# Optimization experiments

Hardware: AMD Instinct MI355X
Metric: run time of the kernel (lower is better)

The kernel has to match this reference:

```python
import jax, jax.numpy as jnp
import numpy as np

EMB = 4096   # emb_size for c2=256 (per TransformerEncoderBlock mapping)
HEADS = 16
HDIM = EMB // HEADS  # 256
N = 25               # (h // (h//5))**2 patches
PATCH = 4            # h//5 with h=20
C = 256
HW = 20
LN_EPS = 1e-5


def _layernorm(x, g, b):
    m = jnp.mean(x, axis=-1, keepdims=True)
    v = jnp.var(x, axis=-1, keepdims=True)
    return (x - m) * jax.lax.rsqrt(v + LN_EPS) * g + b


def setup_inputs() -> dict:
    key = jax.random.key(0)
    ks = jax.random.split(key, 14)
    s = 0.02
    rn = lambda k, shape, sc=s: jax.random.normal(k, shape, jnp.float32) * sc
    return {
        "x": jax.random.normal(ks[0], (1, C, HW, HW), jnp.float32),
        # PatchEmbedding: Conv2d(C, EMB, k=4, s=4) + positions
        "pe_w": rn(ks[1], (EMB, C, PATCH, PATCH)),
        "pe_b": jnp.zeros((EMB,), jnp.float32),
        "pos": rn(ks[2], (N, EMB), 1.0),  # nn.Parameter(torch.randn(...))
        # shared LayerNorm (same module used twice per block)
        "ln_g": jnp.ones((EMB,), jnp.float32),
        "ln_b": jnp.zeros((EMB,), jnp.float32),
        # attention
        "qkv_w": rn(ks[3], (EMB, 3 * EMB)),
        "qkv_b": jnp.zeros((3 * EMB,), jnp.float32),
        "proj_w": rn(ks[4], (EMB, EMB)),
        "proj_b": jnp.zeros((EMB,), jnp.float32),
        # FFN (expansion 4)
        "ff1_w": rn(ks[5], (EMB, 4 * EMB)),
        "ff1_b": jnp.zeros((4 * EMB,), jnp.float32),
        "ff2_w": rn(ks[6], (4 * EMB, EMB)),
        "ff2_b": jnp.zeros((EMB,), jnp.float32),
    }


def _forward(x, pe_w, pe_b, pos, ln_g, ln_b, qkv_w, qkv_b, proj_w, proj_b,
             ff1_w, ff1_b, ff2_w, ff2_b):
    b = x.shape[0]
    # Patch embedding: Conv2d(k=4, s=4) -> [b, EMB, 5, 5] -> [b, 25, EMB]
    t = jax.lax.conv_general_dilated(
        x, pe_w, window_strides=(PATCH, PATCH), padding="VALID",
        dimension_numbers=("NCHW", "OIHW", "NCHW"))
    t = t + pe_b[None, :, None, None]
    t = t.reshape(b, EMB, N).transpose(0, 2, 1) + pos  # [b, N, EMB]

    # --- TransformerEncoderBlock (dropout inactive / eval mode) ---
    # attention branch
    h = _layernorm(t, ln_g, ln_b)
    qkv = (h @ qkv_w + qkv_b).reshape(b, N, HEADS, HDIM, 3)  # (h d qkv) split
    q = qkv[..., 0].transpose(0, 2, 1, 3)  # [b, H, N, D]
    k = qkv[..., 1].transpose(0, 2, 1, 3)
    v = qkv[..., 2].transpose(0, 2, 1, 3)
    energy = jnp.einsum("bhqd,bhkd->bhqk", q, k)
    # NOTE: original scales AFTER softmax by sqrt(emb_size) -- faithful copy
    att = jax.nn.softmax(energy, axis=-1) / (EMB ** 0.5)
    o = jnp.einsum("bhqk,bhkd->bhqd", att, v)
    o = o.transpose(0, 2, 1, 3).reshape(b, N, EMB)
    t = t + (o @ proj_w + proj_b)

    # FFN branch (same shared layernorm params)
    h = _layernorm(t, ln_g, ln_b)
    h = jax.nn.gelu(h @ ff1_w + ff1_b, approximate=False)  # torch nn.GELU exact
    t = t + (h @ ff2_w + ff2_b)

    # final reshape(1, c2, w, h)
    return t.reshape(1, C, HW, HW)


def reference(x, pe_w, pe_b, pos, ln_g, ln_b, qkv_w, qkv_b, proj_w, proj_b,
              ff1_w, ff1_b, ff2_w, ff2_b):
    return _forward(x, pe_w, pe_b, pos, ln_g, ln_b, qkv_w, qkv_b, proj_w,
                    proj_b, ff1_w, ff1_b, ff2_w, ff2_b)
```

## Files before the change

### kernel.cpp

```cpp
#include <hip/hip_runtime.h>
#include <math.h>

#define TOK 25

typedef __attribute__((ext_vector_type(8))) short short8_t;
typedef __attribute__((ext_vector_type(4))) float f32x4_t;
typedef __attribute__((ext_vector_type(8))) float floatx8;
typedef __attribute__((ext_vector_type(4))) float floatx4;
typedef __attribute__((ext_vector_type(8))) __bf16 bf16x8_t;
typedef __attribute__((ext_vector_type(4))) __bf16 bf16x4_t;

__device__ __forceinline__ short8_t cvt8(floatx8 f) {
  return __builtin_bit_cast(short8_t, __builtin_convertvector(f, bf16x8_t));
}
__device__ __forceinline__ uint2 cvt4pack(float4 v) {
  floatx4 f = {v.x, v.y, v.z, v.w};
  return __builtin_bit_cast(uint2, __builtin_convertvector(f, bf16x4_t));
}
__device__ __forceinline__ uint2 pack4(f32x4_t v) {
  floatx4 f = {v[0], v[1], v[2], v[3]};
  return __builtin_bit_cast(uint2, __builtin_convertvector(f, bf16x4_t));
}
__device__ __forceinline__ unsigned short bf1(float f) {
  return __builtin_bit_cast(unsigned short, (__bf16)f);
}


template <int KC, int WT, int G, int D>
__global__ __launch_bounds__(256) void k_mfma(
    const unsigned short* __restrict__ A, const float* __restrict__ W,
    uint2* __restrict__ part, int K, int N) {
  constexpr int LDA = KC + 8;
  constexpr int NS = KC / 32;
  __shared__ __align__(16) unsigned short As[TOK * LDA];
  const int tid = threadIdx.x;
  const int lane = tid & 63;
  const int lm = lane & 15;
  const int lg = lane >> 4;
  const int wv = tid >> 6;
  const int s = blockIdx.y;
  const int k0 = s * KC;
  const int c0 = blockIdx.x * (64 * G) + wv * (16 * G);
  for (int i = tid; i < TOK * (KC / 8); i += 256) {
    int r = i / (KC / 8);
    int o = i - r * (KC / 8);
    uint4 v = *reinterpret_cast<const uint4*>(A + (long)r * K + k0 + o * 8);
    *reinterpret_cast<uint4*>(&As[r * LDA + o * 8]) = v;
  }
  __syncthreads();
  const int r1 = 16 + lm;
  const int r1c = (r1 < TOK) ? r1 : 0;
  f32x4_t acc[G][2];
#pragma unroll
  for (int g = 0; g < G; ++g) {
    acc[g][0] = (f32x4_t){0.f, 0.f, 0.f, 0.f};
    acc[g][1] = (f32x4_t){0.f, 0.f, 0.f, 0.f};
  }
  auto loadW = [&](int ks, floatx8(&dst)[G]) {
    const int kb = k0 + ks + lg * 8;
    if (WT == 0) {
      const float* bp = W + (long)kb * N + c0 + lm;
#pragma unroll
      for (int j = 0; j < 8; ++j) {
        const float* bj = bp + (long)j * N;
#pragma unroll
        for (int g = 0; g < G; ++g) dst[g][j] = bj[g * 16];
      }
    } else {
#pragma unroll
      for (int g = 0; g < G; ++g) {
        const float* bp = W + (long)(c0 + g * 16 + lm) * K + kb;
        float4 b0 = *reinterpret_cast<const float4*>(bp);
        float4 b1 = *reinterpret_cast<const float4*>(bp + 4);
        dst[g] = (floatx8){b0.x, b0.y, b0.z, b0.w, b1.x, b1.y, b1.z, b1.w};
      }
    }
  };
  floatx8 wb[D + 1][G];
  loadW(0, wb[0]);
  if (D >= 2 && NS > 1) loadW(32, wb[1 % (D + 1)]);
#pragma unroll
  for (int st = 0; st < NS; ++st) {
    if (st + D < NS) loadW((st + D) * 32, wb[(st + D) % (D + 1)]);
    short8_t av0 =
        *reinterpret_cast<const short8_t*>(&As[lm * LDA + st * 32 + lg * 8]);
    short8_t av1 =
        *reinterpret_cast<const short8_t*>(&As[r1c * LDA + st * 32 + lg * 8]);
#pragma unroll
    for (int g = 0; g < G; ++g) {
      short8_t bv = cvt8(wb[st % (D + 1)][g]);
      acc[g][0] = __builtin_amdgcn_mfma_f32_16x16x32_bf16(av0, bv, acc[g][0], 0, 0, 0);
      acc[g][1] = __builtin_amdgcn_mfma_f32_16x16x32_bf16(av1, bv, acc[g][1], 0, 0, 0);
    }
  }
  const long sbase = (long)s * N * 8;
#pragma unroll
  for (int g = 0; g < G; ++g) {
    long t = ((long)(c0 >> 4) + g) * 128;
    part[sbase + t + lane] = pack4(acc[g][0]);
    part[sbase + t + 64 + lane] = pack4(acc[g][1]);
  }
}

template <int KC, int G, int D>
__global__ __launch_bounds__(256) void k_mfma_pe(
    const float* __restrict__ x, const float* __restrict__ W,
    uint2* __restrict__ part, int K, int N) {
  constexpr int LDA = KC + 8;
  constexpr int NS = KC / 32;
  __shared__ __align__(16) unsigned short As[TOK * LDA];
  const int tid = threadIdx.x;
  const int lane = tid & 63;
  const int lm = lane & 15;
  const int lg = lane >> 4;
  const int wv = tid >> 6;
  const int s = blockIdx.y;
  const int k0 = s * KC;
  const int c0 = blockIdx.x * (64 * G) + wv * (16 * G);
  for (int i = tid; i < TOK * (KC / 8); i += 256) {
    int r = i / (KC / 8);
    int o = i - r * (KC / 8);
    int kb = k0 + o * 8;
    int c = kb >> 4;
    int kh0 = (kb >> 2) & 3;
    int py = r / 5, px = r - py * 5;
    const float* xp = x + c * 400 + (py * 4 + kh0) * 20 + px * 4;
    float4 lo = *reinterpret_cast<const float4*>(xp);
    float4 hi = *reinterpret_cast<const float4*>(xp + 20);
    floatx8 f = {lo.x, lo.y, lo.z, lo.w, hi.x, hi.y, hi.z, hi.w};
    *reinterpret_cast<short8_t*>(&As[r * LDA + o * 8]) = cvt8(f);
  }
  __syncthreads();
  const int r1 = 16 + lm;
  const int r1c = (r1 < TOK) ? r1 : 0;
  f32x4_t acc[G][2];
#pragma unroll
  for (int g = 0; g < G; ++g) {
    acc[g][0] = (f32x4_t){0.f, 0.f, 0.f, 0.f};
    acc[g][1] = (f32x4_t){0.f, 0.f, 0.f, 0.f};
  }
  auto loadW = [&](int ks, floatx8(&dst)[G]) {
    const int kb = k0 + ks + lg * 8;
#pragma unroll
    for (int g = 0; g < G; ++g) {
      const float* bp = W + (long)(c0 + g * 16 + lm) * K + kb;
      float4 b0 = *reinterpret_cast<const float4*>(bp);
      float4 b1 = *reinterpret_cast<const float4*>(bp + 4);
      dst[g] = (floatx8){b0.x, b0.y, b0.z, b0.w, b1.x, b1.y, b1.z, b1.w};
    }
  };
  floatx8 wb[D + 1][G];
  loadW(0, wb[0]);
  if (D >= 2 && NS > 1) loadW(32, wb[1 % (D + 1)]);
#pragma unroll
  for (int st = 0; st < NS; ++st) {
    if (st + D < NS) loadW((st + D) * 32, wb[(st + D) % (D + 1)]);
    short8_t av0 =
        *reinterpret_cast<const short8_t*>(&As[lm * LDA + st * 32 + lg * 8]);
    short8_t av1 =
        *reinterpret_cast<const short8_t*>(&As[r1c * LDA + st * 32 + lg * 8]);
#pragma unroll
    for (int g = 0; g < G; ++g) {
      short8_t bv = cvt8(wb[st % (D + 1)][g]);
      acc[g][0] = __builtin_amdgcn_mfma_f32_16x16x32_bf16(av0, bv, acc[g][0], 0, 0, 0);
      acc[g][1] = __builtin_amdgcn_mfma_f32_16x16x32_bf16(av1, bv, acc[g][1], 0, 0, 0);
    }
  }
  const long sbase = (long)s * N * 8;
#pragma unroll
  for (int g = 0; g < G; ++g) {
    long t = ((long)(c0 >> 4) + g) * 128;
    part[sbase + t + lane] = pack4(acc[g][0]);
    part[sbase + t + 64 + lane] = pack4(acc[g][1]);
  }
}

template <int S, int GELU, int RES, int OBF>
__global__ __launch_bounds__(128) void k_reduce(const uint2* __restrict__ part,
                                                const float* __restrict__ bias,
                                                const float* __restrict__ res,
                                                void* __restrict__ outv,
                                                int Nout) {
  const long gidx = (long)blockIdx.x * 128 + threadIdx.x;
  const int lane = (int)(gidx & 63);
  const int half = (int)((gidx >> 6) & 1);
  const long ct = gidx >> 7;
  const int lm = lane & 15, lg = lane >> 4;
  const int col = (int)(ct * 16 + lm);
  const long stride = (long)Nout * 8;
  const uint2* pp = part + gidx;
  float a[4] = {0.f, 0.f, 0.f, 0.f};
#pragma unroll 16
  for (int s = 0; s < S; ++s) {
    uint2 u = pp[(long)s * stride];
    a[0] += __builtin_bit_cast(float, (u.x & 0xffffu) << 16);
    a[1] += __builtin_bit_cast(float, u.x & 0xffff0000u);
    a[2] += __builtin_bit_cast(float, (u.y & 0xffffu) << 16);
    a[3] += __builtin_bit_cast(float, u.y & 0xffff0000u);
  }
  const float bb = bias[col];
#pragma unroll
  for (int r = 0; r < 4; ++r) {
    a[r] += bb;
    if (GELU) a[r] = 0.5f * a[r] * (1.f + erff(a[r] * 0.70710678118654752f));
  }
  const int row0 = half * 16 + lg * 4;
#pragma unroll
  for (int r = 0; r < 4; ++r) {
    int row = row0 + r;
    if (row < TOK) {
      float v = a[r];
      if (RES) v += res[(long)row * Nout + col];
      if (OBF) {
        ((unsigned short*)outv)[(long)row * Nout + col] = bf1(v);
      } else {
        ((float*)outv)[(long)row * Nout + col] = v;
      }
    }
  }
}

__global__ __launch_bounds__(256) void k_ln(const float* __restrict__ t,
                                            const float* __restrict__ g,
                                            const float* __restrict__ b,
                                            unsigned short* __restrict__ h) {
  const int n = blockIdx.x;
  const float4* row = reinterpret_cast<const float4*>(t + n * 4096);
  float s = 0.f, s2 = 0.f;
  float4 vbuf[4];
#pragma unroll
  for (int it = 0; it < 4; ++it) {
    float4 v = row[threadIdx.x + it * 256];
    vbuf[it] = v;
    s += v.x + v.y + v.z + v.w;
    s2 += v.x * v.x + v.y * v.y + v.z * v.z + v.w * v.w;
  }
#pragma unroll
  for (int off = 32; off >= 1; off >>= 1) {
    s += __shfl_down(s, off);
    s2 += __shfl_down(s2, off);
  }
  __shared__ float red[8];
  if ((threadIdx.x & 63) == 0) {
    red[threadIdx.x >> 6] = s;
    red[4 + (threadIdx.x >> 6)] = s2;
  }
  __syncthreads();
  float st = red[0] + red[1] + red[2] + red[3];
  float s2t = red[4] + red[5] + red[6] + red[7];
  float mean = st * (1.f / 4096.f);
  float var = s2t * (1.f / 4096.f) - mean * mean;
  float rstd = rsqrtf(var + 1e-5f);
  const float4* g4 = reinterpret_cast<const float4*>(g);
  const float4* b4 = reinterpret_cast<const float4*>(b);
  uint2* h2 = reinterpret_cast<uint2*>(h) + (long)n * 1024;
#pragma unroll
  for (int it = 0; it < 4; ++it) {
    int i = threadIdx.x + it * 256;
    float4 v = vbuf[it];
    float4 gg = g4[i];
    float4 bb = b4[i];
    float4 o;
    o.x = (v.x - mean) * rstd * gg.x + bb.x;
    o.y = (v.y - mean) * rstd * gg.y + bb.y;
    o.z = (v.z - mean) * rstd * gg.z + bb.z;
    o.w = (v.w - mean) * rstd * gg.w + bb.w;
    h2[i] = cvt4pack(o);
  }
}

__global__ __launch_bounds__(256) void k_attn(const float* __restrict__ qkv,
                                              unsigned short* __restrict__ o) {
  const int head = blockIdx.x;
  __shared__ float q[TOK][260];
  __shared__ float kk[TOK][260];
  __shared__ float att[TOK][TOK];
  const int d = threadIdx.x;
#pragma unroll
  for (int n = 0; n < TOK; ++n) {
    const long base = (long)n * 12288 + (head * 256 + d) * 3;
    q[n][d] = qkv[base];
    kk[n][d] = qkv[base + 1];
  }
  __syncthreads();
  for (int p = threadIdx.x; p < TOK * TOK; p += 256) {
    int i = p / TOK, j = p - i * TOK;
    float acc = 0.f;
#pragma unroll
    for (int c = 0; c < 256; c += 4) {
      float4 a = *reinterpret_cast<const float4*>(&q[i][c]);
      float4 bb = *reinterpret_cast<const float4*>(&kk[j][c]);
      acc = fmaf(a.x, bb.x, acc);
      acc = fmaf(a.y, bb.y, acc);
      acc = fmaf(a.z, bb.z, acc);
      acc = fmaf(a.w, bb.w, acc);
    }
    att[i][j] = acc;
  }
  __syncthreads();
  if (threadIdx.x < TOK) {
    const int i = threadIdx.x;
    float m = -1e30f;
    for (int j = 0; j < TOK; ++j) m = fmaxf(m, att[i][j]);
    float ssum = 0.f;
    float ex[TOK];
#pragma unroll
    for (int j = 0; j < TOK; ++j) {
      ex[j] = expf(att[i][j] - m);
      ssum += ex[j];
    }
    float inv = 1.f / (ssum * 64.f);
#pragma unroll
    for (int j = 0; j < TOK; ++j) att[i][j] = ex[j] * inv;
  }
  __syncthreads();
  float acc[TOK];
#pragma unroll
  for (int i = 0; i < TOK; ++i) acc[i] = 0.f;
#pragma unroll
  for (int j = 0; j < TOK; ++j) {
    float vv = qkv[(long)j * 12288 + (head * 256 + d) * 3 + 2];
#pragma unroll
    for (int i = 0; i < TOK; ++i) acc[i] = fmaf(att[i][j], vv, acc[i]);
  }
#pragma unroll
  for (int i = 0; i < TOK; ++i)
    o[(long)i * 4096 + head * 256 + d] = bf1(acc[i]);
}

extern "C" void kernel_launch(void* const* d_in, const int* in_sizes, int n_in,
                              void* d_out, int out_size, void* d_ws, size_t ws_size,
                              hipStream_t stream) {
  (void)in_sizes; (void)n_in; (void)out_size; (void)ws_size;
  const float* x      = (const float*)d_in[0];
  const float* pe_w   = (const float*)d_in[1];
  const float* pe_b   = (const float*)d_in[2];
  const float* pos    = (const float*)d_in[3];
  const float* ln_g   = (const float*)d_in[4];
  const float* ln_b   = (const float*)d_in[5];
  const float* qkv_w  = (const float*)d_in[6];
  const float* qkv_b  = (const float*)d_in[7];
  const float* proj_w = (const float*)d_in[8];
  const float* proj_b = (const float*)d_in[9];
  const float* ff1_w  = (const float*)d_in[10];
  const float* ff1_b  = (const float*)d_in[11];
  const float* ff2_w  = (const float*)d_in[12];
  const float* ff2_b  = (const float*)d_in[13];
  float* out = (float*)d_out;

  float* ws = (float*)d_ws;
  float* T    = ws + 102400;
  unsigned short* H_bf = (unsigned short*)(ws + 204800);
  float* QKV  = ws + 307200;
  unsigned short* O_bf = (unsigned short*)(ws + 614400);
  unsigned short* G_bf = (unsigned short*)(ws + 716800);
  uint2* PART = (uint2*)(ws + 1136400);

  k_mfma_pe<128, 2, 2><<<dim3(32, 32), 256, 0, stream>>>(x, pe_w, PART, 4096, 4096);
  k_reduce<32, 0, 1, 0><<<256, 128, 0, stream>>>(PART, pe_b, pos, T, 4096);
  k_ln<<<25, 256, 0, stream>>>(T, ln_g, ln_b, H_bf);

  k_mfma<256, 0, 2, 2><<<dim3(96, 16), 256, 0, stream>>>(H_bf, qkv_w, PART, 4096, 12288);
  k_reduce<16, 0, 0, 0><<<768, 128, 0, stream>>>(PART, qkv_b, nullptr, QKV, 12288);
  k_attn<<<16, 256, 0, stream>>>(QKV, O_bf);
  k_mfma<128, 0, 2, 2><<<dim3(32, 32), 256, 0, stream>>>(O_bf, proj_w, PART, 4096, 4096);
  k_reduce<32, 0, 1, 0><<<256, 128, 0, stream>>>(PART, proj_b, T, T, 4096);
  k_ln<<<25, 256, 0, stream>>>(T, ln_g, ln_b, H_bf);

  k_mfma<256, 0, 4, 1><<<dim3(64, 16), 256, 0, stream>>>(H_bf, ff1_w, PART, 4096, 16384);
  k_reduce<16, 1, 0, 1><<<1024, 128, 0, stream>>>(PART, ff1_b, nullptr, G_bf, 16384);
  k_mfma<512, 0, 2, 2><<<dim3(32, 32), 256, 0, stream>>>(G_bf, ff2_w, PART, 16384, 4096);
  k_reduce<32, 0, 1, 0><<<256, 128, 0, stream>>>(PART, ff2_b, T, out, 4096);
}
```

Baseline: 229.8 us.

## Fuse split-K reductions into GEMM kernels via last-block atomic counter

Removes the separate k_reduce launches by having each split-K GEMM block atomically increment a per-column-tile counter, with the last arriving block summing all partials and applying bias, GELU and residual. Partials are written and read with agent-scope relaxed atomics so the finalizing block sees them. The aim is to cut kernel launch overhead and inter-kernel gaps, at the cost of an added memset, serial reduction work on the last block of each column tile, and atomic traffic.

```diff
diff --git a/kernel.cpp b/kernel.cpp
--- a/kernel.cpp
+++ b/kernel.cpp
@@ -17,22 +17,85 @@
   floatx4 f = {v.x, v.y, v.z, v.w};
   return __builtin_bit_cast(uint2, __builtin_convertvector(f, bf16x4_t));
 }
-__device__ __forceinline__ uint2 pack4(f32x4_t v) {
+__device__ __forceinline__ unsigned long long pack4ull(f32x4_t v) {
   floatx4 f = {v[0], v[1], v[2], v[3]};
-  return __builtin_bit_cast(uint2, __builtin_convertvector(f, bf16x4_t));
+  return __builtin_bit_cast(unsigned long long,
+                            __builtin_convertvector(f, bf16x4_t));
 }
 __device__ __forceinline__ unsigned short bf1(float f) {
   return __builtin_bit_cast(unsigned short, (__bf16)f);
 }
 
 
-template <int KC, int WT, int G, int D>
+__device__ __forceinline__ void store_part(uint2* p, unsigned long long v) {
+  __hip_atomic_store((unsigned long long*)p, v, __ATOMIC_RELAXED,
+                     __HIP_MEMORY_SCOPE_AGENT);
+}
+__device__ __forceinline__ uint2 load_part(const uint2* p) {
+  unsigned long long raw = __hip_atomic_load(
+      (const unsigned long long*)p, __ATOMIC_RELAXED, __HIP_MEMORY_SCOPE_AGENT);
+  return __builtin_bit_cast(uint2, raw);
+}
+
+template <int G, int S, int GELU, int RES, int OBF>
+__device__ __forceinline__ void k_finalize(const uint2* __restrict__ part,
+                                           const float* __restrict__ bias,
+                                           const float* __restrict__ res,
+                                           void* __restrict__ outv, int bx,
+                                           int N, int tid) {
+  const long base = (long)bx * (G * 4) * 128;
+  const long stride = (long)N * 8;
+#pragma unroll
+  for (int it = 0; it < 2 * G; ++it) {
+    long p = base + (long)it * 256 + tid;
+    int lane = (int)(p & 63);
+    int half = (int)((p >> 6) & 1);
+    long ct = p >> 7;
+    int lm = lane & 15, lg = lane >> 4;
+    int col = (int)(ct * 16 + lm);
+    const uint2* pp = part + p;
+    float a[4] = {0.f, 0.f, 0.f, 0.f};
+#pragma unroll 8
+    for (int s = 0; s < S; ++s) {
+      uint2 u = load_part(&pp[(long)s * stride]);
+      a[0] += __builtin_bit_cast(float, (u.x & 0xffffu) << 16);
+      a[1] += __builtin_bit_cast(float, u.x & 0xffff0000u);
+      a[2] += __builtin_bit_cast(float, (u.y & 0xffffu) << 16);
+      a[3] += __builtin_bit_cast(float, u.y & 0xffff0000u);
+    }
+    const float bb = bias[col];
+#pragma unroll
+    for (int r = 0; r < 4; ++r) {
+      a[r] += bb;
+      if (GELU) a[r] = 0.5f * a[r] * (1.f + erff(a[r] * 0.70710678118654752f));
+    }
+    const int row0 = half * 16 + lg * 4;
+#pragma unroll
+    for (int r = 0; r < 4; ++r) {
+      int row = row0 + r;
+      if (row < TOK) {
+        float v = a[r];
+        if (RES) v += res[(long)row * N + col];
+        if (OBF) {
+          ((unsigned short*)outv)[(long)row * N + col] = bf1(v);
+        } else {
+          ((float*)outv)[(long)row * N + col] = v;
+        }
+      }
+    }
+  }
+}
+
+template <int KC, int WT, int G, int D, int S, int GELU, int RES, int OBF>
 __global__ __launch_bounds__(256) void k_mfma(
     const unsigned short* __restrict__ A, const float* __restrict__ W,
-    uint2* __restrict__ part, int K, int N) {
+    uint2* __restrict__ part, const float* __restrict__ bias,
+    const float* __restrict__ res, void* __restrict__ outv,
+    int* __restrict__ cnt, int K, int N) {
   constexpr int LDA = KC + 8;
   constexpr int NS = KC / 32;
   __shared__ __align__(16) unsigned short As[TOK * LDA];
+  __shared__ int doit;
   const int tid = threadIdx.x;
   const int lane = tid & 63;
   const int lm = lane & 15;
@@ -97,18 +160,29 @@
 #pragma unroll
   for (int g = 0; g < G; ++g) {
     long t = ((long)(c0 >> 4) + g) * 128;
-    part[sbase + t + lane] = pack4(acc[g][0]);
-    part[sbase + t + 64 + lane] = pack4(acc[g][1]);
-  }
-}
-
-template <int KC, int G, int D>
+    store_part(&part[sbase + t + lane], pack4ull(acc[g][0]));
+    store_part(&part[sbase + t + 64 + lane], pack4ull(acc[g][1]));
+  }
+  if (tid == 0) {
+    int old = __hip_atomic_fetch_add(&cnt[blockIdx.x], 1, __ATOMIC_ACQ_REL,
+                                     __HIP_MEMORY_SCOPE_AGENT);
+    doit = (old == S - 1);
+  }
+  __syncthreads();
+  if (doit) k_finalize<G, S, GELU, RES, OBF>(part, bias, res, outv,
+                                             blockIdx.x, N, tid);
+}
+
+template <int KC, int G, int D, int S>
 __global__ __launch_bounds__(256) void k_mfma_pe(
     const float* __restrict__ x, const float* __restrict__ W,
-    uint2* __restrict__ part, int K, int N) {
+    uint2* __restrict__ part, const float* __restrict__ bias,
+    const float* __restrict__ res, float* __restrict__ outv,
+    int* __restrict__ cnt, int K, int N) {
   constexpr int LDA = KC + 8;
   constexpr int NS = KC / 32;
   __shared__ __align__(16) unsigned short As[TOK * LDA];
+  __shared__ int doit;
   const int tid = threadIdx.x;
   const int lane = tid & 63;
   const int lm = lane & 15;
@@ -170,54 +244,16 @@
 #pragma unroll
   for (int g = 0; g < G; ++g) {
     long t = ((long)(c0 >> 4) + g) * 128;
-    part[sbase + t + lane] = pack4(acc[g][0]);
-    part[sbase + t + 64 + lane] = pack4(acc[g][1]);
-  }
-}
-
-template <int S, int GELU, int RES, int OBF>
-__global__ __launch_bounds__(128) void k_reduce(const uint2* __restrict__ part,
-                                                const float* __restrict__ bias,
-                                                const float* __restrict__ res,
-                                                void* __restrict__ outv,
-                                                int Nout) {
-  const long gidx = (long)blockIdx.x * 128 + threadIdx.x;
-  const int lane = (int)(gidx & 63);
-  const int half = (int)((gidx >> 6) & 1);
-  const long ct = gidx >> 7;
-  const int lm = lane & 15, lg = lane >> 4;
-  const int col = (int)(ct * 16 + lm);
-  const long stride = (long)Nout * 8;
-  const uint2* pp = part + gidx;
-  float a[4] = {0.f, 0.f, 0.f, 0.f};
-#pragma unroll 16
-  for (int s = 0; s < S; ++s) {
-    uint2 u = pp[(long)s * stride];
-    a[0] += __builtin_bit_cast(float, (u.x & 0xffffu) << 16);
-    a[1] += __builtin_bit_cast(float, u.x & 0xffff0000u);
-    a[2] += __builtin_bit_cast(float, (u.y & 0xffffu) << 16);
-    a[3] += __builtin_bit_cast(float, u.y & 0xffff0000u);
-  }
-  const float bb = bias[col];
-#pragma unroll
-  for (int r = 0; r < 4; ++r) {
-    a[r] += bb;
-    if (GELU) a[r] = 0.5f * a[r] * (1.f + erff(a[r] * 0.70710678118654752f));
-  }
-  const int row0 = half * 16 + lg * 4;
-#pragma unroll
-  for (int r = 0; r < 4; ++r) {
-    int row = row0 + r;
-    if (row < TOK) {
-      float v = a[r];
-      if (RES) v += res[(long)row * Nout + col];
-      if (OBF) {
-        ((unsigned short*)outv)[(long)row * Nout + col] = bf1(v);
-      } else {
-        ((float*)outv)[(long)row * Nout + col] = v;
-      }
-    }
-  }
+    store_part(&part[sbase + t + lane], pack4ull(acc[g][0]));
+    store_part(&part[sbase + t + 64 + lane], pack4ull(acc[g][1]));
+  }
+  if (tid == 0) {
+    int old = __hip_atomic_fetch_add(&cnt[blockIdx.x], 1, __ATOMIC_ACQ_REL,
+                                     __HIP_MEMORY_SCOPE_AGENT);
+    doit = (old == S - 1);
+  }
+  __syncthreads();
+  if (doit) k_finalize<G, S, 0, 1, 0>(part, bias, res, outv, blockIdx.x, N, tid);
 }
 
 __global__ __launch_bounds__(256) void k_ln(const float* __restrict__ t,
@@ -354,21 +390,24 @@
   float* QKV  = ws + 307200;
   unsigned short* O_bf = (unsigned short*)(ws + 614400);
   unsigned short* G_bf = (unsigned short*)(ws + 716800);
+  int* CNT = (int*)(ws + 1126400);
   uint2* PART = (uint2*)(ws + 1136400);
 
-  k_mfma_pe<128, 2, 2><<<dim3(32, 32), 256, 0, stream>>>(x, pe_w, PART, 4096, 4096);
-  k_reduce<32, 0, 1, 0><<<256, 128, 0, stream>>>(PART, pe_b, pos, T, 4096);
+  hipMemsetAsync(CNT, 0, 256 * sizeof(int), stream);
+
+  k_mfma_pe<128, 2, 2, 32><<<dim3(32, 32), 256, 0, stream>>>(
+      x, pe_w, PART, pe_b, pos, T, CNT + 0, 4096, 4096);
   k_ln<<<25, 256, 0, stream>>>(T, ln_g, ln_b, H_bf);
 
-  k_mfma<256, 0, 2, 2><<<dim3(96, 16), 256, 0, stream>>>(H_bf, qkv_w, PART, 4096, 12288);
-  k_reduce<16, 0, 0, 0><<<768, 128, 0, stream>>>(PART, qkv_b, nullptr, QKV, 12288);
+  k_mfma<256, 0, 2, 2, 16, 0, 0, 0><<<dim3(96, 16), 256, 0, stream>>>(
+      H_bf, qkv_w, PART, qkv_b, nullptr, QKV, CNT + 32, 4096, 12288);
   k_attn<<<16, 256, 0, stream>>>(QKV, O_bf);
-  k_mfma<128, 0, 2, 2><<<dim3(32, 32), 256, 0, stream>>>(O_bf, proj_w, PART, 4096, 4096);
-  k_reduce<32, 0, 1, 0><<<256, 128, 0, stream>>>(PART, proj_b, T, T, 4096);
+  k_mfma<128, 0, 2, 2, 32, 0, 1, 0><<<dim3(32, 32), 256, 0, stream>>>(
+      O_bf, proj_w, PART, proj_b, T, T, CNT + 128, 4096, 4096);
   k_ln<<<25, 256, 0, stream>>>(T, ln_g, ln_b, H_bf);
 
-  k_mfma<256, 0, 4, 1><<<dim3(64, 16), 256, 0, stream>>>(H_bf, ff1_w, PART, 4096, 16384);
-  k_reduce<16, 1, 0, 1><<<1024, 128, 0, stream>>>(PART, ff1_b, nullptr, G_bf, 16384);
-  k_mfma<512, 0, 2, 2><<<dim3(32, 32), 256, 0, stream>>>(G_bf, ff2_w, PART, 16384, 4096);
-  k_reduce<32, 0, 1, 0><<<256, 128, 0, stream>>>(PART, ff2_b, T, out, 4096);
-}
+  k_mfma<256, 0, 4, 1, 16, 1, 0, 1><<<dim3(64, 16), 256, 0, stream>>>(
+      H_bf, ff1_w, PART, ff1_b, nullptr, G_bf, CNT + 160, 4096, 16384);
+  k_mfma<512, 0, 2, 2, 32, 0, 1, 0><<<dim3(32, 32), 256, 0, stream>>>(
+      G_bf, ff2_w, PART, ff2_b, T, out, CNT + 224, 16384, 4096);
+}
```

New measurement: 541.4 us. 136% more time.
